# Performance work log

Hardware: AMD Instinct MI355X
Metric: run time of the kernel (lower is better)

## Reference

```python
import jax, jax.numpy as jnp
import numpy as np

DIM = 2048
INTER = 1408
N_EXPERTS = 16
TOP_K = 2
N_SHARED = 2
SHARED_INTER = N_SHARED * INTER  # 2816


def setup_inputs() -> dict:
    key = jax.random.key(0)
    ks = jax.random.split(key, 9)
    s = 0.02
    return {
        "x": jax.random.normal(ks[0], (4, 2048, DIM), dtype=jnp.float32),
        "gate_w": jax.random.normal(ks[1], (N_EXPERTS, DIM), dtype=jnp.float32) * s,
        "w1": jax.random.normal(ks[2], (N_EXPERTS, INTER, DIM), dtype=jnp.float32) * s,
        "w2": jax.random.normal(ks[3], (N_EXPERTS, DIM, INTER), dtype=jnp.float32) * s,
        "w3": jax.random.normal(ks[4], (N_EXPERTS, INTER, DIM), dtype=jnp.float32) * s,
        "sw1": jax.random.normal(ks[5], (SHARED_INTER, DIM), dtype=jnp.float32) * s,
        "sw2": jax.random.normal(ks[6], (DIM, SHARED_INTER), dtype=jnp.float32) * s,
        "sw3": jax.random.normal(ks[7], (SHARED_INTER, DIM), dtype=jnp.float32) * s,
    }


def _swiglu(t, wa, wb, wo):
    # t: [T, d_in]; wa, wb: [d_h, d_in]; wo: [d_out, d_h]
    h = jax.nn.silu(t @ wa.T) * (t @ wb.T)
    return h @ wo.T


def reference(x, gate_w, w1, w2, w3, sw1, sw2, sw3):
    shape = x.shape
    t = x.reshape(-1, DIM)                      # [T, dim]
    scores = jax.nn.softmax(t @ gate_w.T, axis=-1)  # [T, E]
    weights, indices = jax.lax.top_k(scores, TOP_K)  # [T, k] each

    y = jnp.zeros_like(t)
    # Small fixed loop over experts (structurally distinct weights).
    # Per-token combine weight for expert e: sum over top-k slots routed to e
    # (matches y[idx] += expert(x[idx]) * weights[idx, top]; zero weight for
    # unrouted tokens reproduces the counts[i]==0 skip exactly).
    for e in range(N_EXPERTS):
        w_e = jnp.sum(jnp.where(indices == e, weights, 0.0), axis=-1)  # [T]
        y = y + _swiglu(t, w1[e], w3[e], w2[e]) * w_e[:, None]

    z = _swiglu(t, sw1, sw3, sw2)               # shared experts MLP
    return (y + z).reshape(shape)
```

## Files before the change

kernel.cpp:

```cpp
#include <hip/hip_runtime.h>
#include <hip/hip_bf16.h>

#define DIM 2048
#define INTER 1408
#define NEXP 16
#define NTOK 8192
#define SINTER 2816

typedef __attribute__((ext_vector_type(8))) short bf16x8;
typedef __attribute__((ext_vector_type(4))) float f32x4;
typedef __attribute__((ext_vector_type(8))) unsigned short u16x8;

__device__ __forceinline__ unsigned short f2bf(float f) {
    union { float f; unsigned u; } a; a.f = f;
    unsigned r = a.u + 0x7fffu + ((a.u >> 16) & 1u);
    return (unsigned short)(r >> 16);
}

__device__ __forceinline__ void gload16(const void* g, void* lds) {
    __builtin_amdgcn_global_load_lds(
        (const __attribute__((address_space(1))) void*)g,
        (__attribute__((address_space(3))) void*)lds, 16, 0, 0);
}

__global__ __launch_bounds__(256) void cast_bf16(const float* __restrict__ s,
                                                 unsigned short* __restrict__ d,
                                                 long long n) {
    long long i = ((long long)blockIdx.x * 256 + threadIdx.x) * 8;
    if (i >= n) return;
    float4 a = *(const float4*)(s + i), b = *(const float4*)(s + i + 4);
    u16x8 o = { f2bf(a.x), f2bf(a.y), f2bf(a.z), f2bf(a.w),
                f2bf(b.x), f2bf(b.y), f2bf(b.z), f2bf(b.w) };
    *(u16x8*)(d + i) = o;
}

__global__ __launch_bounds__(256) void gate_topk(
    const float* __restrict__ x, const float* __restrict__ gw,
    int* __restrict__ counts, int* __restrict__ toklist, float* __restrict__ tokw) {
    int wave = threadIdx.x >> 6;
    int lane = threadIdx.x & 63;
    int tok  = blockIdx.x * 4 + wave;
    const float* xr = x + (size_t)tok * DIM;

    float part[NEXP];
#pragma unroll
    for (int e = 0; e < NEXP; ++e) part[e] = 0.f;
#pragma unroll
    for (int c = 0; c < DIM / 256; ++c) {
        float4 xv = *(const float4*)(xr + c * 256 + lane * 4);
#pragma unroll
        for (int e = 0; e < NEXP; ++e) {
            float4 g = *(const float4*)(gw + e * DIM + c * 256 + lane * 4);
            part[e] += xv.x * g.x + xv.y * g.y + xv.z * g.z + xv.w * g.w;
        }
    }
#pragma unroll
    for (int e = 0; e < NEXP; ++e) {
        float v = part[e];
#pragma unroll
        for (int off = 32; off; off >>= 1) v += __shfl_xor(v, off);
        part[e] = v;
    }
    float mx = part[0];
#pragma unroll
    for (int e = 1; e < NEXP; ++e) mx = fmaxf(mx, part[e]);
    float Z = 0.f;
#pragma unroll
    for (int e = 0; e < NEXP; ++e) Z += expf(part[e] - mx);
    int i1 = 0; float m1 = part[0];
#pragma unroll
    for (int e = 1; e < NEXP; ++e) if (part[e] > m1) { m1 = part[e]; i1 = e; }
    int i2 = -1; float m2 = -1e30f;
#pragma unroll
    for (int e = 0; e < NEXP; ++e) if (e != i1 && part[e] > m2) { m2 = part[e]; i2 = e; }
    if (lane == 0) {
        float w1v = expf(m1 - mx) / Z;
        float w2v = expf(m2 - mx) / Z;
        int p1 = atomicAdd(&counts[i1], 1);
        toklist[i1 * NTOK + p1] = tok; tokw[i1 * NTOK + p1] = w1v;
        int p2 = atomicAdd(&counts[i2], 1);
        toklist[i2 * NTOK + p2] = tok; tokw[i2 * NTOK + p2] = w2v;
    }
}

__global__ void prefix_k(const int* __restrict__ counts, int* __restrict__ base) {
    if (threadIdx.x == 0) {
        int acc = 0;
        for (int e = 0; e < NEXP; ++e) { base[e] = acc; acc += counts[e]; }
        base[16] = acc;
        base[17] = acc + NTOK;
    }
}

__device__ __forceinline__ int swz(int r) { return (r ^ (r >> 2)) & 3; }

__global__ __launch_bounds__(512, 2) void gemm1(
    const unsigned short* __restrict__ xb,
    const unsigned short* __restrict__ w1b, const unsigned short* __restrict__ w3b,
    const unsigned short* __restrict__ sw1b, const unsigned short* __restrict__ sw3b,
    const int* __restrict__ counts, const int* __restrict__ base,
    const int* __restrict__ toklist, unsigned short* __restrict__ hbuf) {
    const int e   = blockIdx.z;
    const int cnt = (e < NEXP) ? counts[e] : NTOK;
    const int m0  = blockIdx.y * 256;
    if (m0 >= cnt) return;
    const int n0  = blockIdx.x * 128;
    const size_t woff = (size_t)((e < NEXP) ? e : e - NEXP) * INTER * DIM;
    const unsigned short* B1 = ((e < NEXP) ? w1b : sw1b) + woff;
    const unsigned short* B3 = ((e < NEXP) ? w3b : sw3b) + woff;
    const int hbase = base[e];
    const int* tl = toklist + e * NTOK;

    __shared__ __attribute__((aligned(16))) unsigned short As[4][8192];
    __shared__ __attribute__((aligned(16))) unsigned short B1s[4][4096];
    __shared__ __attribute__((aligned(16))) unsigned short B3s[4][4096];

    const int tid = threadIdx.x;
    const int w = tid >> 6, l = tid & 63;
    const int wr = w >> 1, wc = w & 1;
    const int lr = l & 15, hi = l >> 4;

    const int row0 = tid >> 2, row1 = row0 + 128;
    const int c0 = (tid & 3) ^ swz(row0);
    int g0 = m0 + row0, g1 = m0 + row1;
    int t0, t1;
    if (e < NEXP) { t0 = (g0 < cnt) ? tl[g0] : 0; t1 = (g1 < cnt) ? tl[g1] : 0; }
    else          { t0 = g0; t1 = g1; }
    const unsigned short* aSrc0 = xb + (size_t)t0 * DIM + c0 * 8;
    const unsigned short* aSrc1 = xb + (size_t)t1 * DIM + c0 * 8;
    const unsigned short* b1Src = B1 + (size_t)(n0 + row0) * DIM + c0 * 8;
    const unsigned short* b3Src = B3 + (size_t)(n0 + row0) * DIM + c0 * 8;

    int aoff[4], boff[4];
#pragma unroll
    for (int m = 0; m < 4; ++m) {
        int r = wr * 64 + m * 16 + lr;
        aoff[m] = r * 64 + ((swz(r) ^ hi) << 4);
    }
#pragma unroll
    for (int n = 0; n < 4; ++n) {
        int r = wc * 64 + n * 16 + lr;
        boff[n] = r * 64 + ((swz(r) ^ hi) << 4);
    }

    f32x4 acc1[4][4], acc3[4][4];
#pragma unroll
    for (int m = 0; m < 4; ++m)
#pragma unroll
        for (int n = 0; n < 4; ++n) {
            acc1[m][n] = (f32x4){0.f, 0.f, 0.f, 0.f};
            acc3[m][n] = (f32x4){0.f, 0.f, 0.f, 0.f};
        }

    const int H = DIM / 32;

    auto STAGE = [&](int hh) {
        int hb = hh & 3;
        int kc = hh * 32;
        gload16(aSrc0 + kc, &As[hb][tid * 8]);
        gload16(aSrc1 + kc, &As[hb][4096 + tid * 8]);
        gload16(b1Src + kc, &B1s[hb][tid * 8]);
        gload16(b3Src + kc, &B3s[hb][tid * 8]);
    };

    STAGE(0); STAGE(1); STAGE(2);
    asm volatile("s_waitcnt vmcnt(8)" ::: "memory");
    __builtin_amdgcn_s_barrier();

    for (int h = 0; h < H; ++h) {
        const int hb = h & 3;
        bf16x8 af[4], b1f[4], b3f[4];
#pragma unroll
        for (int m = 0; m < 4; ++m)
            af[m] = *(const bf16x8*)((const char*)&As[hb][0] + aoff[m]);
#pragma unroll
        for (int n = 0; n < 4; ++n) {
            b1f[n] = *(const bf16x8*)((const char*)&B1s[hb][0] + boff[n]);
            b3f[n] = *(const bf16x8*)((const char*)&B3s[hb][0] + boff[n]);
        }
        if (h + 3 < H) {
            STAGE(h + 3);
            asm volatile("s_waitcnt vmcnt(8)" ::: "memory");
        } else if (h == H - 3) {
            asm volatile("s_waitcnt vmcnt(4)" ::: "memory");
        } else if (h == H - 2) {
            asm volatile("s_waitcnt vmcnt(0)" ::: "memory");
        }
        __builtin_amdgcn_s_barrier();
        asm volatile("s_waitcnt lgkmcnt(0)" ::: "memory");
        __builtin_amdgcn_sched_barrier(0);
        __builtin_amdgcn_s_setprio(1);
#pragma unroll
        for (int m = 0; m < 4; ++m)
#pragma unroll
            for (int n = 0; n < 4; ++n) {
                acc1[m][n] = __builtin_amdgcn_mfma_f32_16x16x32_bf16(af[m], b1f[n], acc1[m][n], 0, 0, 0);
                acc3[m][n] = __builtin_amdgcn_mfma_f32_16x16x32_bf16(af[m], b3f[n], acc3[m][n], 0, 0, 0);
            }
        __builtin_amdgcn_s_setprio(0);
        __builtin_amdgcn_s_barrier();
    }

#pragma unroll
    for (int m = 0; m < 4; ++m) {
#pragma unroll
        for (int i = 0; i < 4; ++i) {
            int row  = wr * 64 + m * 16 + hi * 4 + i;
            int grow = m0 + row;
            if (grow < cnt) {
                size_t ro = (size_t)(hbase + grow) * INTER;
#pragma unroll
                for (int n = 0; n < 4; ++n) {
                    int col = n0 + wc * 64 + n * 16 + lr;
                    float a = acc1[m][n][i];
                    float hv = a / (1.f + __expf(-a)) * acc3[m][n][i];
                    hbuf[ro + col] = f2bf(hv);
                }
            }
        }
    }
}

__global__ __launch_bounds__(512, 2) void gemm2(
    const unsigned short* __restrict__ hbuf,
    const unsigned short* __restrict__ w2b, const unsigned short* __restrict__ sw2b,
    const int* __restrict__ counts, const int* __restrict__ base,
    const int* __restrict__ toklist, const float* __restrict__ tokw,
    float* __restrict__ out) {
    const int e   = blockIdx.z;
    const int cnt = (e < NEXP) ? counts[e] : NTOK;
    const int m0  = blockIdx.y * 256;
    if (m0 >= cnt) return;
    const int n0  = blockIdx.x * 256;
    const int hbase = base[e];
    const size_t bstride = (e < NEXP) ? INTER : SINTER;
    const unsigned short* Bb = (e < NEXP) ? w2b + (size_t)e * DIM * INTER
                                          : sw2b + (size_t)(e - NEXP) * INTER;

    __shared__ __attribute__((aligned(16))) unsigned short Ah[4][8192];
    __shared__ __attribute__((aligned(16))) unsigned short Bh[4][8192];

    const int tid = threadIdx.x;
    const int w = tid >> 6, l = tid & 63;
    const int wr = w >> 2, wc = w & 3;
    const int lr = l & 15, hi = l >> 4;

    const int row0 = tid >> 2, row1 = row0 + 128;
    const int c0 = (tid & 3) ^ swz(row0);
    const unsigned short* aSrc0 = hbuf + (size_t)(hbase + m0 + row0) * INTER + c0 * 8;
    const unsigned short* aSrc1 = hbuf + (size_t)(hbase + m0 + row1) * INTER + c0 * 8;
    const unsigned short* bSrc0 = Bb + (size_t)(n0 + row0) * bstride + c0 * 8;
    const unsigned short* bSrc1 = Bb + (size_t)(n0 + row1) * bstride + c0 * 8;

    int aoff[8], boff[4];
#pragma unroll
    for (int m = 0; m < 8; ++m) {
        int r = wr * 128 + m * 16 + lr;
        aoff[m] = r * 64 + ((swz(r) ^ hi) << 4);
    }
#pragma unroll
    for (int n = 0; n < 4; ++n) {
        int r = wc * 64 + n * 16 + lr;
        boff[n] = r * 64 + ((swz(r) ^ hi) << 4);
    }

    f32x4 acc[8][4];
#pragma unroll
    for (int m = 0; m < 8; ++m)
#pragma unroll
        for (int n = 0; n < 4; ++n) acc[m][n] = (f32x4){0.f, 0.f, 0.f, 0.f};

    const int H = INTER / 32;

    auto STAGE = [&](int hh) {
        int hb = hh & 3;
        int kc = hh * 32;
        gload16(aSrc0 + kc, &Ah[hb][tid * 8]);
        gload16(aSrc1 + kc, &Ah[hb][4096 + tid * 8]);
        gload16(bSrc0 + kc, &Bh[hb][tid * 8]);
        gload16(bSrc1 + kc, &Bh[hb][4096 + tid * 8]);
    };

    STAGE(0); STAGE(1); STAGE(2);
    asm volatile("s_waitcnt vmcnt(8)" ::: "memory");
    __builtin_amdgcn_s_barrier();

    for (int h = 0; h < H; ++h) {
        const int hb = h & 3;
        bf16x8 af[8], bf[4];
#pragma unroll
        for (int m = 0; m < 8; ++m)
            af[m] = *(const bf16x8*)((const char*)&Ah[hb][0] + aoff[m]);
#pragma unroll
        for (int n = 0; n < 4; ++n)
            bf[n] = *(const bf16x8*)((const char*)&Bh[hb][0] + boff[n]);
        if (h + 3 < H) {
            STAGE(h + 3);
            asm volatile("s_waitcnt vmcnt(8)" ::: "memory");
        } else if (h == H - 3) {
            asm volatile("s_waitcnt vmcnt(4)" ::: "memory");
        } else if (h == H - 2) {
            asm volatile("s_waitcnt vmcnt(0)" ::: "memory");
        }
        __builtin_amdgcn_s_barrier();
        asm volatile("s_waitcnt lgkmcnt(0)" ::: "memory");
        __builtin_amdgcn_sched_barrier(0);
        __builtin_amdgcn_s_setprio(1);
#pragma unroll
        for (int m = 0; m < 8; ++m)
#pragma unroll
            for (int n = 0; n < 4; ++n)
                acc[m][n] = __builtin_amdgcn_mfma_f32_16x16x32_bf16(af[m], bf[n], acc[m][n], 0, 0, 0);
        __builtin_amdgcn_s_setprio(0);
        __builtin_amdgcn_s_barrier();
    }

#pragma unroll
    for (int m = 0; m < 8; ++m) {
#pragma unroll
        for (int i = 0; i < 4; ++i) {
            int row  = wr * 128 + m * 16 + hi * 4 + i;
            int grow = m0 + row;
            if (grow < cnt) {
                int tok; float wt;
                if (e < NEXP) { tok = toklist[e * NTOK + grow]; wt = tokw[e * NTOK + grow]; }
                else          { tok = grow; wt = 1.f; }
                float* orow = out + (size_t)tok * DIM + n0 + wc * 64 + lr;
#pragma unroll
                for (int n = 0; n < 4; ++n)
                    unsafeAtomicAdd(orow + n * 16, acc[m][n][i] * wt);
            }
        }
    }
}

extern "C" void kernel_launch(void* const* d_in, const int* in_sizes, int n_in,
                              void* d_out, int out_size, void* d_ws, size_t ws_size,
                              hipStream_t stream) {
    const float* x   = (const float*)d_in[0];
    const float* gw  = (const float*)d_in[1];
    const float* w1  = (const float*)d_in[2];
    const float* w2  = (const float*)d_in[3];
    const float* w3  = (const float*)d_in[4];
    const float* sw1 = (const float*)d_in[5];
    const float* sw2 = (const float*)d_in[6];
    const float* sw3 = (const float*)d_in[7];
    float* out = (float*)d_out;

    char* ws = (char*)d_ws;
    int*   counts  = (int*)ws;
    int*   basep   = (int*)(ws + 128);
    int*   toklist = (int*)(ws + 4096);
    float* tokw    = (float*)(ws + 4096 + (size_t)NEXP * NTOK * 4);
    unsigned short* hbuf = (unsigned short*)(ws + (2u << 20));

    const size_t hbytes = (size_t)4 * NTOK * INTER * 2;
    const size_t offx   = (2ull << 20) + hbytes;
    const size_t xbytes = (size_t)NTOK * DIM * 2;
    const size_t offw   = offx + xbytes;
    const size_t wB     = (size_t)NEXP * INTER * DIM * 2;
    const size_t swB    = (size_t)SINTER * DIM * 2;

    unsigned short* xb   = (unsigned short*)(ws + offx);
    unsigned short* w1b  = (unsigned short*)(ws + offw);
    unsigned short* w3b  = (unsigned short*)(ws + offw + wB);
    unsigned short* w2b  = (unsigned short*)(ws + offw + 2 * wB);
    unsigned short* sw1b = (unsigned short*)(ws + offw + 3 * wB);
    unsigned short* sw3b = (unsigned short*)(ws + offw + 3 * wB + swB);
    unsigned short* sw2b = (unsigned short*)(ws + offw + 3 * wB + 2 * swB);

    hipMemsetAsync(counts, 0, 64, stream);
    hipMemsetAsync(d_out, 0, (size_t)out_size * sizeof(float), stream);

    gate_topk<<<NTOK / 4, 256, 0, stream>>>(x, gw, counts, toklist, tokw);
    prefix_k<<<1, 64, 0, stream>>>(counts, basep);

    auto cast = [&](const float* s, unsigned short* d, long long n) {
        cast_bf16<<<(int)((n / 8 + 255) / 256), 256, 0, stream>>>(s, d, n);
    };
    cast(x, xb, (long long)NTOK * DIM);
    cast(w1, w1b, (long long)NEXP * INTER * DIM);
    cast(w3, w3b, (long long)NEXP * INTER * DIM);
    cast(w2, w2b, (long long)NEXP * INTER * DIM);
    cast(sw1, sw1b, (long long)SINTER * DIM);
    cast(sw3, sw3b, (long long)SINTER * DIM);
    cast(sw2, sw2b, (long long)SINTER * DIM);

    gemm1<<<dim3(INTER / 128, NTOK / 256, 18), 512, 0, stream>>>(
        xb, w1b, w3b, sw1b, sw3b, counts, basep, toklist, hbuf);
    gemm2<<<dim3(DIM / 256, NTOK / 256, 18), 512, 0, stream>>>(
        hbuf, w2b, sw2b, counts, basep, toklist, tokw, out);
}
```

Before: 1.352 ms.

## Fuse x cast into gating, remap GEMM blocks across XCDs, reorder LDS waits

The gating kernel now also writes the bf16 copy of x, so the separate cast pass over x is dropped. Both GEMMs switch to a 1D grid whose block index is remapped so that consecutive blocks of the same expert land on the same XCD, aiming for better L2 reuse of the weight tiles. Inside the main loops the lgkmcnt wait moves after the MFMAs and the MFMA order is changed to run n-major with w1 before w3, so LDS reads can overlap compute. The w2 cast is moved after gemm1. Moving the wait is risky because fragments are consumed before it, and the code depends on the compiler to insert the needed waits.

```diff
diff --git a/kernel.cpp b/kernel.cpp
--- a/kernel.cpp
+++ b/kernel.cpp
@@ -9,7 +9,12 @@
 
 typedef __attribute__((ext_vector_type(8))) short bf16x8;
 typedef __attribute__((ext_vector_type(4))) float f32x4;
+typedef __attribute__((ext_vector_type(4))) unsigned short u16x4;
 typedef __attribute__((ext_vector_type(8))) unsigned short u16x8;
+
+#define VMCNT(n) asm volatile("s_waitcnt vmcnt(" #n ")" ::: "memory")
+#define LGKM0()  asm volatile("s_waitcnt lgkmcnt(0)" ::: "memory")
+#define BARRIER() __builtin_amdgcn_s_barrier()
 
 __device__ __forceinline__ unsigned short f2bf(float f) {
     union { float f; unsigned u; } a; a.f = f;
@@ -36,11 +41,13 @@
 
 __global__ __launch_bounds__(256) void gate_topk(
     const float* __restrict__ x, const float* __restrict__ gw,
+    unsigned short* __restrict__ xb,
     int* __restrict__ counts, int* __restrict__ toklist, float* __restrict__ tokw) {
     int wave = threadIdx.x >> 6;
     int lane = threadIdx.x & 63;
     int tok  = blockIdx.x * 4 + wave;
     const float* xr = x + (size_t)tok * DIM;
+    unsigned short* xbr = xb + (size_t)tok * DIM;
 
     float part[NEXP];
 #pragma unroll
@@ -48,6 +55,8 @@
 #pragma unroll
     for (int c = 0; c < DIM / 256; ++c) {
         float4 xv = *(const float4*)(xr + c * 256 + lane * 4);
+        u16x4 xo = { f2bf(xv.x), f2bf(xv.y), f2bf(xv.z), f2bf(xv.w) };
+        *(u16x4*)(xbr + c * 256 + lane * 4) = xo;
 #pragma unroll
         for (int e = 0; e < NEXP; ++e) {
             float4 g = *(const float4*)(gw + e * DIM + c * 256 + lane * 4);
@@ -100,11 +109,14 @@
     const unsigned short* __restrict__ sw1b, const unsigned short* __restrict__ sw3b,
     const int* __restrict__ counts, const int* __restrict__ base,
     const int* __restrict__ toklist, unsigned short* __restrict__ hbuf) {
-    const int e   = blockIdx.z;
+    const int b = blockIdx.x;
+    const int l = (b & 7) * 792 + (b >> 3);
+    const int e   = l / 352;
+    const int rem = l % 352;
+    const int n0  = (rem >> 5) * 128;
+    const int m0  = (rem & 31) * 256;
     const int cnt = (e < NEXP) ? counts[e] : NTOK;
-    const int m0  = blockIdx.y * 256;
     if (m0 >= cnt) return;
-    const int n0  = blockIdx.x * 128;
     const size_t woff = (size_t)((e < NEXP) ? e : e - NEXP) * INTER * DIM;
     const unsigned short* B1 = ((e < NEXP) ? w1b : sw1b) + woff;
     const unsigned short* B3 = ((e < NEXP) ? w3b : sw3b) + woff;
@@ -116,9 +128,9 @@
     __shared__ __attribute__((aligned(16))) unsigned short B3s[4][4096];
 
     const int tid = threadIdx.x;
-    const int w = tid >> 6, l = tid & 63;
+    const int w = tid >> 6, lu = tid & 63;
     const int wr = w >> 1, wc = w & 1;
-    const int lr = l & 15, hi = l >> 4;
+    const int lr = lu & 15, hi = lu >> 4;
 
     const int row0 = tid >> 2, row1 = row0 + 128;
     const int c0 = (tid & 3) ^ swz(row0);
@@ -164,41 +176,40 @@
     };
 
     STAGE(0); STAGE(1); STAGE(2);
-    asm volatile("s_waitcnt vmcnt(8)" ::: "memory");
-    __builtin_amdgcn_s_barrier();
+    VMCNT(8);
+    BARRIER();
 
     for (int h = 0; h < H; ++h) {
         const int hb = h & 3;
+        const char* As_ = (const char*)&As[hb][0];
+        const char* B1_ = (const char*)&B1s[hb][0];
+        const char* B3_ = (const char*)&B3s[hb][0];
         bf16x8 af[4], b1f[4], b3f[4];
-#pragma unroll
-        for (int m = 0; m < 4; ++m)
-            af[m] = *(const bf16x8*)((const char*)&As[hb][0] + aoff[m]);
-#pragma unroll
-        for (int n = 0; n < 4; ++n) {
-            b1f[n] = *(const bf16x8*)((const char*)&B1s[hb][0] + boff[n]);
-            b3f[n] = *(const bf16x8*)((const char*)&B3s[hb][0] + boff[n]);
-        }
-        if (h + 3 < H) {
-            STAGE(h + 3);
-            asm volatile("s_waitcnt vmcnt(8)" ::: "memory");
-        } else if (h == H - 3) {
-            asm volatile("s_waitcnt vmcnt(4)" ::: "memory");
-        } else if (h == H - 2) {
-            asm volatile("s_waitcnt vmcnt(0)" ::: "memory");
-        }
-        __builtin_amdgcn_s_barrier();
-        asm volatile("s_waitcnt lgkmcnt(0)" ::: "memory");
-        __builtin_amdgcn_sched_barrier(0);
+        b1f[0] = *(const bf16x8*)(B1_ + boff[0]);
+#pragma unroll
+        for (int m = 0; m < 4; ++m) af[m] = *(const bf16x8*)(As_ + aoff[m]);
+#pragma unroll
+        for (int n = 1; n < 4; ++n) b1f[n] = *(const bf16x8*)(B1_ + boff[n]);
+#pragma unroll
+        for (int n = 0; n < 4; ++n) b3f[n] = *(const bf16x8*)(B3_ + boff[n]);
+        if (h + 3 < H) { STAGE(h + 3); VMCNT(8); }
+        else if (h == H - 3) { VMCNT(4); }
+        else if (h == H - 2) { VMCNT(0); }
+        BARRIER();
         __builtin_amdgcn_s_setprio(1);
 #pragma unroll
-        for (int m = 0; m < 4; ++m)
-#pragma unroll
-            for (int n = 0; n < 4; ++n) {
+        for (int n = 0; n < 4; ++n)
+#pragma unroll
+            for (int m = 0; m < 4; ++m)
                 acc1[m][n] = __builtin_amdgcn_mfma_f32_16x16x32_bf16(af[m], b1f[n], acc1[m][n], 0, 0, 0);
+#pragma unroll
+        for (int n = 0; n < 4; ++n)
+#pragma unroll
+            for (int m = 0; m < 4; ++m)
                 acc3[m][n] = __builtin_amdgcn_mfma_f32_16x16x32_bf16(af[m], b3f[n], acc3[m][n], 0, 0, 0);
-            }
         __builtin_amdgcn_s_setprio(0);
-        __builtin_amdgcn_s_barrier();
+        LGKM0();
+        BARRIER();
     }
 
 #pragma unroll
@@ -227,11 +238,14 @@
     const int* __restrict__ counts, const int* __restrict__ base,
     const int* __restrict__ toklist, const float* __restrict__ tokw,
     float* __restrict__ out) {
-    const int e   = blockIdx.z;
+    const int b = blockIdx.x;
+    const int l = (b & 7) * 576 + (b >> 3);
+    const int e   = l / 256;
+    const int rem = l % 256;
+    const int n0  = (rem >> 5) * 256;
+    const int m0  = (rem & 31) * 256;
     const int cnt = (e < NEXP) ? counts[e] : NTOK;
-    const int m0  = blockIdx.y * 256;
     if (m0 >= cnt) return;
-    const int n0  = blockIdx.x * 256;
     const int hbase = base[e];
     const size_t bstride = (e < NEXP) ? INTER : SINTER;
     const unsigned short* Bb = (e < NEXP) ? w2b + (size_t)e * DIM * INTER
@@ -241,9 +255,9 @@
     __shared__ __attribute__((aligned(16))) unsigned short Bh[4][8192];
 
     const int tid = threadIdx.x;
-    const int w = tid >> 6, l = tid & 63;
+    const int w = tid >> 6, lu = tid & 63;
     const int wr = w >> 2, wc = w & 3;
-    const int lr = l & 15, hi = l >> 4;
+    const int lr = lu & 15, hi = lu >> 4;
 
     const int row0 = tid >> 2, row1 = row0 + 128;
     const int c0 = (tid & 3) ^ swz(row0);
@@ -282,37 +296,32 @@
     };
 
     STAGE(0); STAGE(1); STAGE(2);
-    asm volatile("s_waitcnt vmcnt(8)" ::: "memory");
-    __builtin_amdgcn_s_barrier();
+    VMCNT(8);
+    BARRIER();
 
     for (int h = 0; h < H; ++h) {
         const int hb = h & 3;
+        const char* A_ = (const char*)&Ah[hb][0];
+        const char* B_ = (const char*)&Bh[hb][0];
         bf16x8 af[8], bf[4];
-#pragma unroll
-        for (int m = 0; m < 8; ++m)
-            af[m] = *(const bf16x8*)((const char*)&Ah[hb][0] + aoff[m]);
+        bf[0] = *(const bf16x8*)(B_ + boff[0]);
+#pragma unroll
+        for (int m = 0; m < 8; ++m) af[m] = *(const bf16x8*)(A_ + aoff[m]);
+#pragma unroll
+        for (int n = 1; n < 4; ++n) bf[n] = *(const bf16x8*)(B_ + boff[n]);
+        if (h + 3 < H) { STAGE(h + 3); VMCNT(8); }
+        else if (h == H - 3) { VMCNT(4); }
+        else if (h == H - 2) { VMCNT(0); }
+        BARRIER();
+        __builtin_amdgcn_s_setprio(1);
 #pragma unroll
         for (int n = 0; n < 4; ++n)
-            bf[n] = *(const bf16x8*)((const char*)&Bh[hb][0] + boff[n]);
-        if (h + 3 < H) {
-            STAGE(h + 3);
-            asm volatile("s_waitcnt vmcnt(8)" ::: "memory");
-        } else if (h == H - 3) {
-            asm volatile("s_waitcnt vmcnt(4)" ::: "memory");
-        } else if (h == H - 2) {
-            asm volatile("s_waitcnt vmcnt(0)" ::: "memory");
-        }
-        __builtin_amdgcn_s_barrier();
-        asm volatile("s_waitcnt lgkmcnt(0)" ::: "memory");
-        __builtin_amdgcn_sched_barrier(0);
-        __builtin_amdgcn_s_setprio(1);
-#pragma unroll
-        for (int m = 0; m < 8; ++m)
-#pragma unroll
-            for (int n = 0; n < 4; ++n)
+#pragma unroll
+            for (int m = 0; m < 8; ++m)
                 acc[m][n] = __builtin_amdgcn_mfma_f32_16x16x32_bf16(af[m], bf[n], acc[m][n], 0, 0, 0);
         __builtin_amdgcn_s_setprio(0);
-        __builtin_amdgcn_s_barrier();
+        LGKM0();
+        BARRIER();
     }
 
 #pragma unroll
@@ -372,22 +381,23 @@
     hipMemsetAsync(counts, 0, 64, stream);
     hipMemsetAsync(d_out, 0, (size_t)out_size * sizeof(float), stream);
 
-    gate_topk<<<NTOK / 4, 256, 0, stream>>>(x, gw, counts, toklist, tokw);
+    gate_topk<<<NTOK / 4, 256, 0, stream>>>(x, gw, xb, counts, toklist, tokw);
     prefix_k<<<1, 64, 0, stream>>>(counts, basep);
 
     auto cast = [&](const float* s, unsigned short* d, long long n) {
         cast_bf16<<<(int)((n / 8 + 255) / 256), 256, 0, stream>>>(s, d, n);
     };
-    cast(x, xb, (long long)NTOK * DIM);
     cast(w1, w1b, (long long)NEXP * INTER * DIM);
     cast(w3, w3b, (long long)NEXP * INTER * DIM);
-    cast(w2, w2b, (long long)NEXP * INTER * DIM);
     cast(sw1, sw1b, (long long)SINTER * DIM);
     cast(sw3, sw3b, (long long)SINTER * DIM);
+
+    gemm1<<<18 * 11 * 32, 512, 0, stream>>>(
+        xb, w1b, w3b, sw1b, sw3b, counts, basep, toklist, hbuf);
+
+    cast(w2, w2b, (long long)NEXP * INTER * DIM);
     cast(sw2, sw2b, (long long)SINTER * DIM);
 
-    gemm1<<<dim3(INTER / 128, NTOK / 256, 18), 512, 0, stream>>>(
-        xb, w1b, w3b, sw1b, sw3b, counts, basep, toklist, hbuf);
-    gemm2<<<dim3(DIM / 256, NTOK / 256, 18), 512, 0, stream>>>(
+    gemm2<<<18 * 8 * 32, 512, 0, stream>>>(
         hbuf, w2b, sw2b, counts, basep, toklist, tokw, out);
 }
```

After: 2.897 ms. +114.2%, slower.
